# Kernel optimization log

Measured on AMD Instinct MI355X. Metric: run time of the kernel, lower is better.

## Reference

```python
import jax, jax.numpy as jnp
import numpy as np

L = 16          # n_levels
F = 2           # n_features_per_level
LOG2_T = 19
T = 1 << LOG2_T # hashmap size per level
BASE_RES = 16
FINEST_RES = 2048
_b = (FINEST_RES / BASE_RES) ** (1.0 / (L - 1))
RES = [int(np.floor(BASE_RES * _b ** l)) for l in range(L)]
PRIMES = (1, 2654435761, 805459861, 3674653429)
H = 2 * L * F   # 64 = n_neurons (static 32 + dynamic 32)
N_PTS = 2097152


def hash_encode(coords, table):
    """Multi-resolution hash grid encoding. coords [N,D] in [0,1], table [L,T,F] -> [N, L*F]."""
    N, D = coords.shape
    # 2^D corner offsets of the enclosing grid cell
    offsets = np.stack(
        np.meshgrid(*([np.array([0, 1], dtype=np.uint32)] * D), indexing='ij'), -1
    ).reshape(-1, D)
    primes = [jnp.uint32(p) for p in PRIMES[:D]]
    feats = []
    for l in range(L):  # fixed small loop over levels
        pos = coords * RES[l]
        grid = jnp.floor(pos)
        frac = pos - grid                       # [N,D] interpolation weights
        gu = grid.astype(jnp.int32).astype(jnp.uint32)
        acc = jnp.zeros((N, F), coords.dtype)
        for off in offsets:                     # fixed 2^D corners
            idx = gu + off[None, :]
            h = idx[:, 0] * primes[0]
            for d in range(1, D):
                h = h ^ (idx[:, d] * primes[d])
            h = (h & jnp.uint32(T - 1)).astype(jnp.int32)
            w = jnp.prod(jnp.where(off[None, :] != 0, frac, 1.0 - frac), axis=1)
            acc = acc + w[:, None] * table[l, h]
        feats.append(acc)
    return jnp.concatenate(feats, -1)


def setup_inputs() -> dict:
    key = jax.random.key(0)
    ks = jax.random.split(key, 12)
    s = 1.0 / np.sqrt(H)
    return {
        'x': jax.random.uniform(ks[0], (N_PTS, 3), jnp.float32),
        't': jax.random.uniform(ks[1], (), jnp.float32),
        'table_static': jax.random.uniform(ks[2], (L, T, F), jnp.float32, -1e-4, 1e-4),
        'table_dynamic': jax.random.uniform(ks[3], (L, T, F), jnp.float32, -1e-4, 1e-4),
        'w1_0': jax.random.normal(ks[4], (H, H), jnp.float32) * s,
        'w1_1': jax.random.normal(ks[5], (H, H), jnp.float32) * s,
        'w1_2': jax.random.normal(ks[6], (H, H), jnp.float32) * s,
        'w2_0': jax.random.normal(ks[7], (H, H), jnp.float32) * s,
        'w2_1': jax.random.normal(ks[8], (H, H), jnp.float32) * s,
        'w2_2': jax.random.normal(ks[9], (H, 1), jnp.float32) * s,
        'skip_alpha': jnp.float32(0.5),
    }


def reference(x, t, table_static, table_dynamic, w1_0, w1_1, w1_2,
              w2_0, w2_1, w2_2, skip_alpha):
    relu = jax.nn.relu
    # t_input = cat([x, full((N,1), t)])
    t_col = jnp.broadcast_to(t.astype(x.dtype), (x.shape[0], 1))
    t_input = jnp.concatenate([x, t_col], axis=1)
    static_features = hash_encode(x, table_static)          # [N,32]
    dynamic_features = hash_encode(t_input, table_dynamic)  # [N,32]
    feat = jnp.concatenate([static_features, dynamic_features], -1)  # [N,64]
    # net_1: 2 hidden layers, ReLU everywhere incl. output activation
    h = relu(feat @ w1_0)
    h = relu(h @ w1_1)
    out1 = relu(h @ w1_2)
    # adaptive skip blend
    blend = out1 * skip_alpha + (1.0 - skip_alpha) * feat
    # net_2: 2 hidden layers ReLU, linear output -> [N,1]
    h = relu(blend @ w2_0)
    h = relu(h @ w2_1)
    return h @ w2_2
```

## Files before the change

kernel.cpp:

```cpp
#include <hip/hip_runtime.h>
#include <math.h>

#define LVLS 16
#define TMASK ((1u << 19) - 1u)
#define NT 256
#define TSLICE (1u << 20)
#define KPL (1u << 19)

typedef _Float16 h4 __attribute__((ext_vector_type(4)));
typedef short bf8i __attribute__((ext_vector_type(8)));
typedef float f4 __attribute__((ext_vector_type(4)));

#define ESCALE 1024.0f
#define EINV   0.0009765625f

struct ResParams { float rf[LVLS]; };

__device__ __forceinline__ unsigned hash3(unsigned ux, unsigned uy, unsigned uz) {
    return ux ^ (uy * 2654435761u) ^ (uz * 805459861u);
}

__device__ __forceinline__ unsigned short bf16_rne(float f) {
    unsigned u = __builtin_bit_cast(unsigned, f);
    unsigned r = (u + 0x7FFFu + ((u >> 16) & 1u)) >> 16;
    return (unsigned short)r;
}
__device__ __forceinline__ float bf16_to_f(unsigned short h) {
    unsigned u = ((unsigned)h) << 16;
    return __builtin_bit_cast(float, u);
}

__device__ __forceinline__ void split8t(const float* v, bf8i& h, bf8i& l) {
    unsigned H[4], L[4];
    #pragma unroll
    for (int p = 0; p < 4; ++p) {
        const unsigned u0 = __builtin_bit_cast(unsigned, v[2 * p]);
        const unsigned u1 = __builtin_bit_cast(unsigned, v[2 * p + 1]);
        const unsigned h0 = u0 & 0xffff0000u;
        const unsigned h1 = u1 & 0xffff0000u;
        const float l0 = v[2 * p]     - __builtin_bit_cast(float, h0);
        const float l1 = v[2 * p + 1] - __builtin_bit_cast(float, h1);
        H[p] = (u0 >> 16) | h1;
        L[p] = (__builtin_bit_cast(unsigned, l0) >> 16)
             | (__builtin_bit_cast(unsigned, l1) & 0xffff0000u);
    }
    uint4 Hv = make_uint4(H[0], H[1], H[2], H[3]);
    uint4 Lv = make_uint4(L[0], L[1], L[2], L[3]);
    h = __builtin_bit_cast(bf8i, Hv);
    l = __builtin_bit_cast(bf8i, Lv);
}

__global__ __launch_bounds__(NT, 8)
void build_E(const float* __restrict__ tabs, const float* __restrict__ tabd,
             const float* __restrict__ t_ptr, h4* __restrict__ E, ResParams rp)
{
    const unsigned idx = blockIdx.x * NT + threadIdx.x;
    const unsigned l = idx >> 19;
    const unsigned k = idx & TMASK;
    const float r = rp.rf[l];
    const float tt = t_ptr[0];
    const float ft = tt * r;
    const float gt = floorf(ft);
    const float wt = ft - gt;
    const unsigned ut = (unsigned)(int)gt;
    const unsigned c0 = (ut * 3674653429u) & TMASK;
    const unsigned c1 = ((ut + 1u) * 3674653429u) & TMASK;
    const float* ts = tabs + (size_t)l * TSLICE;
    const float* td = tabd + (size_t)l * TSLICE;
    const float2 s  = *(const float2*)(ts + (size_t)k * 2u);
    const float2 d0 = *(const float2*)(td + (size_t)(k ^ c0) * 2u);
    const float2 d1 = *(const float2*)(td + (size_t)(k ^ c1) * 2u);
    const float om = 1.f - wt;
    h4 v;
    v.x = (_Float16)(s.x * ESCALE);
    v.y = (_Float16)(s.y * ESCALE);
    v.z = (_Float16)((om * d0.x + wt * d1.x) * ESCALE);
    v.w = (_Float16)((om * d0.y + wt * d1.y) * ESCALE);
    E[idx] = v;
}

__global__ __launch_bounds__(NT)
void build_W(const float* __restrict__ w10, const float* __restrict__ w11,
             const float* __restrict__ w12, const float* __restrict__ w20,
             const float* __restrict__ w21, const float* __restrict__ w22,
             unsigned short* __restrict__ Wf)
{
    const int tid = blockIdx.x * NT + threadIdx.x;
    if (tid >= 6 * 4 * 2 * 64) return;
    const int lane = tid & 63;
    const int ks = (tid >> 6) & 1;
    const int nt = (tid >> 7) & 3;
    const int L  = tid >> 9;
    const int g = lane >> 4, c = lane & 15;
    unsigned short* dst = Wf + (size_t)tid * 16;
    #pragma unroll
    for (int j = 0; j < 8; ++j) {
        const int k = ks * 32 + g * 8 + j;
        float v;
        if      (L == 0) v = w10[k * 64 + nt * 16 + c];
        else if (L == 1) v = w11[k * 64 + nt * 16 + c];
        else if (L == 2) v = w12[k * 64 + nt * 16 + c];
        else if (L == 3) v = w20[k * 64 + nt * 16 + c];
        else if (L == 4) v = w21[k * 64 + nt * 16 + c];
        else             v = (nt == 0 && c == 0) ? w22[k] : 0.f;
        unsigned short hb = bf16_rne(v);
        unsigned short lb = bf16_rne(v - bf16_to_f(hb));
        dst[j]     = hb;
        dst[8 + j] = lb;
    }
}

__global__ __launch_bounds__(NT, 8)
void enc_all(const float* __restrict__ x, const h4* __restrict__ E,
             h4* __restrict__ fb, long cp, int npts, ResParams rp)
{
    const int b = blockIdx.x;
    const int l = b & 15;
    const int gid = (b >> 4) * NT + threadIdx.x;
    if (gid >= npts) return;
    const float r = rp.rf[l];
    const h4* Es = E + (size_t)l * KPL;

    const float px = x[3 * gid + 0];
    const float py = x[3 * gid + 1];
    const float pz = x[3 * gid + 2];
    const float fx = px * r, fy = py * r, fz = pz * r;
    const float gx = floorf(fx), gy = floorf(fy), gz = floorf(fz);
    const float wx = fx - gx, wy = fy - gy, wz = fz - gz;
    const unsigned ux = (unsigned)(int)gx;
    const unsigned uy = (unsigned)(int)gy;
    const unsigned uz = (unsigned)(int)gz;
    float a0 = 0.f, a1 = 0.f, b0 = 0.f, b1 = 0.f;
    #pragma unroll
    for (int cc = 0; cc < 8; ++cc) {
        const unsigned ox = (cc >> 2) & 1, oy = (cc >> 1) & 1, oz = cc & 1;
        const unsigned kk = hash3(ux + ox, uy + oy, uz + oz) & TMASK;
        const float w = (ox ? wx : 1.f - wx)
                      * (oy ? wy : 1.f - wy)
                      * (oz ? wz : 1.f - wz);
        const h4 e = Es[kk];
        a0 = fmaf(w, (float)e.x, a0);
        a1 = fmaf(w, (float)e.y, a1);
        b0 = fmaf(w, (float)e.z, b0);
        b1 = fmaf(w, (float)e.w, b1);
    }
    h4 v;
    v.x = (_Float16)a0;
    v.y = (_Float16)a1;
    v.z = (_Float16)b0;
    v.w = (_Float16)b1;
    __builtin_nontemporal_store(__builtin_bit_cast(unsigned long long, v),
                                (unsigned long long*)&fb[(size_t)l * cp + gid]);
}

#define MLPT 128
__global__ __launch_bounds__(MLPT)
void mlp_mfma(const h4* __restrict__ fb, long cp, const uint4* __restrict__ Wf,
              const float* __restrict__ alpha_ptr, float* __restrict__ out, int npts)
{
    __shared__ float XBs[2][64 * 68];
    const int lane = threadIdx.x & 63;
    const int wv   = threadIdx.x >> 6;
    const int base = blockIdx.x * MLPT + wv * 64;
    if (base >= npts) return;
    float* xb = XBs[wv];
    const int g = lane >> 4, c = lane & 15;
    const float alpha = alpha_ptr[0];
    const float oma = 1.f - alpha;

    bf8i ah[4][2], al[4][2];

    #pragma unroll
    for (int mt = 0; mt < 4; ++mt) {
        float t0[8], t1[8];
        #pragma unroll
        for (int jj = 0; jj < 4; ++jj) {
            const h4 e = fb[(size_t)(g * 4 + jj) * cp + base + mt * 16 + c];
            t0[2 * jj] = (float)e.x; t0[2 * jj + 1] = (float)e.y;
            t1[2 * jj] = (float)e.z; t1[2 * jj + 1] = (float)e.w;
        }
        split8t(t0, ah[mt][0], al[mt][0]);
        split8t(t1, ah[mt][1], al[mt][1]);
    }

    auto run_layer = [&](int Lidx, bool relu) {
        #pragma unroll
        for (int nt = 0; nt < 4; ++nt) {
            const uint4* wp0 = Wf + ((size_t)(((Lidx * 4 + nt) * 2 + 0) * 64 + lane)) * 2;
            const uint4* wp1 = Wf + ((size_t)(((Lidx * 4 + nt) * 2 + 1) * 64 + lane)) * 2;
            const bf8i wh0 = __builtin_bit_cast(bf8i, wp0[0]);
            const bf8i wl0 = __builtin_bit_cast(bf8i, wp0[1]);
            const bf8i wh1 = __builtin_bit_cast(bf8i, wp1[0]);
            const bf8i wl1 = __builtin_bit_cast(bf8i, wp1[1]);
            f4 acc[4];
            #pragma unroll
            for (int mt = 0; mt < 4; ++mt) acc[mt] = (f4){0.f, 0.f, 0.f, 0.f};
            #pragma unroll
            for (int mt = 0; mt < 4; ++mt)
                acc[mt] = __builtin_amdgcn_mfma_f32_16x16x32_bf16(ah[mt][0], wh0, acc[mt], 0, 0, 0);
            #pragma unroll
            for (int mt = 0; mt < 4; ++mt)
                acc[mt] = __builtin_amdgcn_mfma_f32_16x16x32_bf16(ah[mt][1], wh1, acc[mt], 0, 0, 0);
            #pragma unroll
            for (int mt = 0; mt < 4; ++mt)
                acc[mt] = __builtin_amdgcn_mfma_f32_16x16x32_bf16(ah[mt][0], wl0, acc[mt], 0, 0, 0);
            #pragma unroll
            for (int mt = 0; mt < 4; ++mt)
                acc[mt] = __builtin_amdgcn_mfma_f32_16x16x32_bf16(ah[mt][1], wl1, acc[mt], 0, 0, 0);
            #pragma unroll
            for (int mt = 0; mt < 4; ++mt)
                acc[mt] = __builtin_amdgcn_mfma_f32_16x16x32_bf16(al[mt][0], wh0, acc[mt], 0, 0, 0);
            #pragma unroll
            for (int mt = 0; mt < 4; ++mt)
                acc[mt] = __builtin_amdgcn_mfma_f32_16x16x32_bf16(al[mt][1], wh1, acc[mt], 0, 0, 0);
            #pragma unroll
            for (int mt = 0; mt < 4; ++mt)
              #pragma unroll
              for (int r = 0; r < 4; ++r) {
                float v = acc[mt][r];
                if (relu) v = fmaxf(v, 0.f);
                xb[(mt * 16 + g * 4 + r) * 68 + nt * 16 + c] = v;
              }
        }
    };

    auto load_frags = [&](bool blend) {
        asm volatile("s_waitcnt lgkmcnt(0)" ::: "memory");
        #pragma unroll
        for (int mt = 0; mt < 4; ++mt) {
            float t0[8], t1[8];
            #pragma unroll
            for (int j = 0; j < 8; ++j) t0[j] = xb[(mt * 16 + c) * 68 + g * 8 + j];
            #pragma unroll
            for (int j = 0; j < 8; ++j) t1[j] = xb[(mt * 16 + c) * 68 + 32 + g * 8 + j];
            if (blend) {
                #pragma unroll
                for (int jj = 0; jj < 4; ++jj) {
                    const h4 e = fb[(size_t)(g * 4 + jj) * cp + base + mt * 16 + c];
                    t0[2 * jj]     = fmaf(t0[2 * jj],     alpha, oma * (float)e.x);
                    t0[2 * jj + 1] = fmaf(t0[2 * jj + 1], alpha, oma * (float)e.y);
                    t1[2 * jj]     = fmaf(t1[2 * jj],     alpha, oma * (float)e.z);
                    t1[2 * jj + 1] = fmaf(t1[2 * jj + 1], alpha, oma * (float)e.w);
                }
            }
            split8t(t0, ah[mt][0], al[mt][0]);
            split8t(t1, ah[mt][1], al[mt][1]);
        }
        asm volatile("s_waitcnt lgkmcnt(0)" ::: "memory");
    };

    run_layer(0, true);
    load_frags(false);
    run_layer(1, true);
    load_frags(false);
    run_layer(2, true);
    load_frags(true);
    run_layer(3, true);
    load_frags(false);
    run_layer(4, true);
    load_frags(false);

    {
        const uint4* wp0 = Wf + ((size_t)(((5 * 4 + 0) * 2 + 0) * 64 + lane)) * 2;
        const uint4* wp1 = Wf + ((size_t)(((5 * 4 + 0) * 2 + 1) * 64 + lane)) * 2;
        const bf8i wh0 = __builtin_bit_cast(bf8i, wp0[0]);
        const bf8i wl0 = __builtin_bit_cast(bf8i, wp0[1]);
        const bf8i wh1 = __builtin_bit_cast(bf8i, wp1[0]);
        const bf8i wl1 = __builtin_bit_cast(bf8i, wp1[1]);
        f4 acc[4];
        #pragma unroll
        for (int mt = 0; mt < 4; ++mt) acc[mt] = (f4){0.f, 0.f, 0.f, 0.f};
        #pragma unroll
        for (int mt = 0; mt < 4; ++mt)
            acc[mt] = __builtin_amdgcn_mfma_f32_16x16x32_bf16(ah[mt][0], wh0, acc[mt], 0, 0, 0);
        #pragma unroll
        for (int mt = 0; mt < 4; ++mt)
            acc[mt] = __builtin_amdgcn_mfma_f32_16x16x32_bf16(ah[mt][1], wh1, acc[mt], 0, 0, 0);
        #pragma unroll
        for (int mt = 0; mt < 4; ++mt)
            acc[mt] = __builtin_amdgcn_mfma_f32_16x16x32_bf16(ah[mt][0], wl0, acc[mt], 0, 0, 0);
        #pragma unroll
        for (int mt = 0; mt < 4; ++mt)
            acc[mt] = __builtin_amdgcn_mfma_f32_16x16x32_bf16(ah[mt][1], wl1, acc[mt], 0, 0, 0);
        #pragma unroll
        for (int mt = 0; mt < 4; ++mt)
            acc[mt] = __builtin_amdgcn_mfma_f32_16x16x32_bf16(al[mt][0], wh0, acc[mt], 0, 0, 0);
        #pragma unroll
        for (int mt = 0; mt < 4; ++mt)
            acc[mt] = __builtin_amdgcn_mfma_f32_16x16x32_bf16(al[mt][1], wh1, acc[mt], 0, 0, 0);
        if (c == 0) {
            #pragma unroll
            for (int mt = 0; mt < 4; ++mt) {
                float4 st = make_float4(acc[mt][0] * EINV, acc[mt][1] * EINV,
                                        acc[mt][2] * EINV, acc[mt][3] * EINV);
                *reinterpret_cast<float4*>(&out[base + mt * 16 + g * 4]) = st;
            }
        }
    }
}

__global__ __launch_bounds__(NT, 2)
void hashmlp_fused(const float* __restrict__ x, const float* __restrict__ t_ptr,
                   const float* __restrict__ tab_s, const float* __restrict__ tab_d,
                   const float* __restrict__ w10, const float* __restrict__ w11,
                   const float* __restrict__ w12, const float* __restrict__ w20,
                   const float* __restrict__ w21, const float* __restrict__ w22,
                   const float* __restrict__ alpha_ptr, float* __restrict__ out,
                   int n, ResParams rp)
{
    __shared__ float smem[64 * NT];
    const int tid = threadIdx.x;
    const int gid = blockIdx.x * NT + tid;
    if (gid >= n) return;
    const float px = x[3 * gid], py = x[3 * gid + 1], pz = x[3 * gid + 2];
    const float tt = t_ptr[0];
    const float alpha = alpha_ptr[0];
    float feat[64];
    #pragma unroll
    for (int l = 0; l < LVLS; ++l) {
        const float r = rp.rf[l];
        const float fx = px * r, fy = py * r, fz = pz * r;
        const float gx = floorf(fx), gy = floorf(fy), gz = floorf(fz);
        const float wx = fx - gx, wy = fy - gy, wz = fz - gz;
        const unsigned ux = (unsigned)(int)gx, uy = (unsigned)(int)gy, uz = (unsigned)(int)gz;
        const float* tb = tab_s + ((size_t)l << 20);
        float a0 = 0.f, a1 = 0.f;
        #pragma unroll
        for (int cc = 0; cc < 8; ++cc) {
            const unsigned ox = (cc >> 2) & 1, oy = (cc >> 1) & 1, oz = cc & 1;
            const unsigned idx = hash3(ux + ox, uy + oy, uz + oz) & TMASK;
            const float w = (ox ? wx : 1.f - wx) * (oy ? wy : 1.f - wy) * (oz ? wz : 1.f - wz);
            const float2 f = *reinterpret_cast<const float2*>(tb + ((size_t)idx * 2u));
            a0 = fmaf(w, f.x, a0); a1 = fmaf(w, f.y, a1);
        }
        feat[2 * l] = a0; feat[2 * l + 1] = a1;
    }
    #pragma unroll
    for (int l = 0; l < LVLS; ++l) {
        const float r = rp.rf[l];
        const float fx = px * r, fy = py * r, fz = pz * r;
        const float gx = floorf(fx), gy = floorf(fy), gz = floorf(fz);
        const float wx = fx - gx, wy = fy - gy, wz = fz - gz;
        const unsigned ux = (unsigned)(int)gx, uy = (unsigned)(int)gy, uz = (unsigned)(int)gz;
        const float ftp = tt * r;
        const float gt = floorf(ftp);
        const float wtp = ftp - gt;
        const unsigned ut = (unsigned)(int)gt;
        const unsigned ht0 = ut * 3674653429u;
        const unsigned ht1 = (ut + 1u) * 3674653429u;
        const float* tb = tab_d + ((size_t)l << 20);
        float a0 = 0.f, a1 = 0.f;
        #pragma unroll
        for (int cc = 0; cc < 8; ++cc) {
            const unsigned ox = (cc >> 2) & 1, oy = (cc >> 1) & 1, oz = cc & 1;
            const unsigned hs = hash3(ux + ox, uy + oy, uz + oz);
            const float ws = (ox ? wx : 1.f - wx) * (oy ? wy : 1.f - wy) * (oz ? wz : 1.f - wz);
            {
                const unsigned idx = (hs ^ ht0) & TMASK;
                const float w = ws * (1.f - wtp);
                const float2 f = *reinterpret_cast<const float2*>(tb + ((size_t)idx * 2u));
                a0 = fmaf(w, f.x, a0); a1 = fmaf(w, f.y, a1);
            }
            {
                const unsigned idx = (hs ^ ht1) & TMASK;
                const float w = ws * wtp;
                const float2 f = *reinterpret_cast<const float2*>(tb + ((size_t)idx * 2u));
                a0 = fmaf(w, f.x, a0); a1 = fmaf(w, f.y, a1);
            }
        }
        feat[32 + 2 * l] = a0; feat[33 + 2 * l] = a1;
    }
    #pragma unroll
    for (int i = 0; i < 64; ++i) smem[i * NT + tid] = feat[i];
    float acc[64];
    auto layer = [&](const float* __restrict__ W, bool do_relu) {
        #pragma unroll
        for (int j = 0; j < 64; ++j) acc[j] = 0.f;
        for (int i = 0; i < 64; ++i) {
            const float fi = smem[i * NT + tid];
            const float* wr = W + i * 64;
            #pragma unroll
            for (int j = 0; j < 64; ++j) acc[j] = fmaf(fi, wr[j], acc[j]);
        }
        #pragma unroll
        for (int j = 0; j < 64; ++j) {
            const float v = do_relu ? fmaxf(acc[j], 0.f) : acc[j];
            smem[j * NT + tid] = v;
        }
    };
    layer(w10, true); layer(w11, true); layer(w12, true);
    #pragma unroll
    for (int j = 0; j < 64; ++j) {
        const float o1 = smem[j * NT + tid];
        smem[j * NT + tid] = fmaf(o1, alpha, (1.f - alpha) * feat[j]);
    }
    layer(w20, true); layer(w21, true);
    float o = 0.f;
    for (int i = 0; i < 64; ++i) o = fmaf(smem[i * NT + tid], w22[i], o);
    out[gid] = o;
}

extern "C" void kernel_launch(void* const* d_in, const int* in_sizes, int n_in,
                              void* d_out, int out_size, void* d_ws, size_t ws_size,
                              hipStream_t stream) {
    (void)n_in; (void)out_size;
    const float* x     = (const float*)d_in[0];
    const float* t     = (const float*)d_in[1];
    const float* tabs  = (const float*)d_in[2];
    const float* tabd  = (const float*)d_in[3];
    const float* w10   = (const float*)d_in[4];
    const float* w11   = (const float*)d_in[5];
    const float* w12   = (const float*)d_in[6];
    const float* w20   = (const float*)d_in[7];
    const float* w21   = (const float*)d_in[8];
    const float* w22   = (const float*)d_in[9];
    const float* alpha = (const float*)d_in[10];
    float* out = (float*)d_out;
    const int n = in_sizes[0] / 3;

    ResParams rp;
    const double b = pow(2048.0 / 16.0, 1.0 / 15.0);
    for (int l = 0; l < LVLS; ++l)
        rp.rf[l] = (float)(int)floor(16.0 * pow(b, (double)l));

    const size_t E_BYTES = (size_t)LVLS * KPL * 8u;
    const size_t W_BYTES = 128u * 1024u;
    if (ws_size < E_BYTES + W_BYTES + 256u * 1024u) {
        dim3 grid((n + NT - 1) / NT), block(NT);
        hipLaunchKernelGGL(hashmlp_fused, grid, block, 0, stream,
                           x, t, tabs, tabd, w10, w11, w12, w20, w21, w22,
                           alpha, out, n, rp);
        return;
    }

    h4* E = (h4*)d_ws;
    unsigned short* Wf = (unsigned short*)((char*)d_ws + E_BYTES);
    h4* fb = (h4*)((char*)d_ws + E_BYTES + W_BYTES);
    long cp_cap = (long)((ws_size - E_BYTES - W_BYTES) / 128u) & ~255L;
    long cp = cp_cap < (long)n ? cp_cap : (long)n;

    {
        const unsigned total = LVLS * KPL;
        hipLaunchKernelGGL(build_E, dim3(total / NT), dim3(NT), 0, stream,
                           tabs, tabd, t, E, rp);
        hipLaunchKernelGGL(build_W, dim3(12), dim3(NT), 0, stream,
                           w10, w11, w12, w20, w21, w22, Wf);
    }

    for (long start = 0; start < n; start += cp) {
        const long m = (n - start) < cp ? (n - start) : cp;
        const unsigned ptb = (unsigned)((m + NT - 1) / NT);
        hipLaunchKernelGGL(enc_all, dim3(ptb * 16), dim3(NT), 0, stream,
                           x + 3 * start, E, fb, cp, (int)m, rp);
        dim3 mgrid((unsigned)((m + MLPT - 1) / MLPT));
        hipLaunchKernelGGL(mlp_mfma, mgrid, dim3(MLPT), 0, stream,
                           fb, cp, (const uint4*)Wf, alpha, out + start, (int)m);
    }
}
```

Before: 1.673 ms.

## Process MLP rows in half tiles to shrink LDS; launch encoding level-major

The MLP layer loop now processes the 64-row wave tile in two 32-row halves. After each half it writes activations to a smaller per-wave LDS buffer and reloads fragments, which halves shared memory per block and adds a min-blocks launch bound to raise occupancy. The encode kernel switches from interleaving levels in blockIdx.x to a 2D grid with the level in blockIdx.y. That makes consecutive blocks share a level, which changes hash-table cache locality: better per-level L2 reuse, but possibly worse reuse of x. Splitting into halves adds extra waitcnt syncs and may shorten MFMA dependency chains.

```diff
diff --git a/kernel.cpp b/kernel.cpp
--- a/kernel.cpp
+++ b/kernel.cpp
@@ -114,9 +114,8 @@
 void enc_all(const float* __restrict__ x, const h4* __restrict__ E,
              h4* __restrict__ fb, long cp, int npts, ResParams rp)
 {
-    const int b = blockIdx.x;
-    const int l = b & 15;
-    const int gid = (b >> 4) * NT + threadIdx.x;
+    const int l = blockIdx.y;
+    const int gid = blockIdx.x * NT + threadIdx.x;
     if (gid >= npts) return;
     const float r = rp.rf[l];
     const h4* Es = E + (size_t)l * KPL;
@@ -154,11 +153,11 @@
 }
 
 #define MLPT 128
-__global__ __launch_bounds__(MLPT)
+__global__ __launch_bounds__(MLPT, 4)
 void mlp_mfma(const h4* __restrict__ fb, long cp, const uint4* __restrict__ Wf,
               const float* __restrict__ alpha_ptr, float* __restrict__ out, int npts)
 {
-    __shared__ float XBs[2][64 * 68];
+    __shared__ float XBs[2][32 * 68];
     const int lane = threadIdx.x & 63;
     const int wv   = threadIdx.x >> 6;
     const int base = blockIdx.x * MLPT + wv * 64;
@@ -183,82 +182,69 @@
         split8t(t1, ah[mt][1], al[mt][1]);
     }
 
-    auto run_layer = [&](int Lidx, bool relu) {
-        #pragma unroll
-        for (int nt = 0; nt < 4; ++nt) {
-            const uint4* wp0 = Wf + ((size_t)(((Lidx * 4 + nt) * 2 + 0) * 64 + lane)) * 2;
-            const uint4* wp1 = Wf + ((size_t)(((Lidx * 4 + nt) * 2 + 1) * 64 + lane)) * 2;
-            const bf8i wh0 = __builtin_bit_cast(bf8i, wp0[0]);
-            const bf8i wl0 = __builtin_bit_cast(bf8i, wp0[1]);
-            const bf8i wh1 = __builtin_bit_cast(bf8i, wp1[0]);
-            const bf8i wl1 = __builtin_bit_cast(bf8i, wp1[1]);
-            f4 acc[4];
+    auto layer = [&](int Lidx, bool blend) {
+        #pragma unroll
+        for (int half = 0; half < 2; ++half) {
+            const int m0 = 2 * half, m1 = 2 * half + 1;
             #pragma unroll
-            for (int mt = 0; mt < 4; ++mt) acc[mt] = (f4){0.f, 0.f, 0.f, 0.f};
-            #pragma unroll
-            for (int mt = 0; mt < 4; ++mt)
-                acc[mt] = __builtin_amdgcn_mfma_f32_16x16x32_bf16(ah[mt][0], wh0, acc[mt], 0, 0, 0);
-            #pragma unroll
-            for (int mt = 0; mt < 4; ++mt)
-                acc[mt] = __builtin_amdgcn_mfma_f32_16x16x32_bf16(ah[mt][1], wh1, acc[mt], 0, 0, 0);
-            #pragma unroll
-            for (int mt = 0; mt < 4; ++mt)
-                acc[mt] = __builtin_amdgcn_mfma_f32_16x16x32_bf16(ah[mt][0], wl0, acc[mt], 0, 0, 0);
-            #pragma unroll
-            for (int mt = 0; mt < 4; ++mt)
-                acc[mt] = __builtin_amdgcn_mfma_f32_16x16x32_bf16(ah[mt][1], wl1, acc[mt], 0, 0, 0);
-            #pragma unroll
-            for (int mt = 0; mt < 4; ++mt)
-                acc[mt] = __builtin_amdgcn_mfma_f32_16x16x32_bf16(al[mt][0], wh0, acc[mt], 0, 0, 0);
-            #pragma unroll
-            for (int mt = 0; mt < 4; ++mt)
-                acc[mt] = __builtin_amdgcn_mfma_f32_16x16x32_bf16(al[mt][1], wh1, acc[mt], 0, 0, 0);
-            #pragma unroll
-            for (int mt = 0; mt < 4; ++mt)
-              #pragma unroll
-              for (int r = 0; r < 4; ++r) {
-                float v = acc[mt][r];
-                if (relu) v = fmaxf(v, 0.f);
-                xb[(mt * 16 + g * 4 + r) * 68 + nt * 16 + c] = v;
-              }
-        }
-    };
-
-    auto load_frags = [&](bool blend) {
-        asm volatile("s_waitcnt lgkmcnt(0)" ::: "memory");
-        #pragma unroll
-        for (int mt = 0; mt < 4; ++mt) {
-            float t0[8], t1[8];
-            #pragma unroll
-            for (int j = 0; j < 8; ++j) t0[j] = xb[(mt * 16 + c) * 68 + g * 8 + j];
-            #pragma unroll
-            for (int j = 0; j < 8; ++j) t1[j] = xb[(mt * 16 + c) * 68 + 32 + g * 8 + j];
-            if (blend) {
+            for (int nt = 0; nt < 4; ++nt) {
+                const uint4* wp0 = Wf + ((size_t)(((Lidx * 4 + nt) * 2 + 0) * 64 + lane)) * 2;
+                const uint4* wp1 = Wf + ((size_t)(((Lidx * 4 + nt) * 2 + 1) * 64 + lane)) * 2;
+                const bf8i wh0 = __builtin_bit_cast(bf8i, wp0[0]);
+                const bf8i wl0 = __builtin_bit_cast(bf8i, wp0[1]);
+                const bf8i wh1 = __builtin_bit_cast(bf8i, wp1[0]);
+                const bf8i wl1 = __builtin_bit_cast(bf8i, wp1[1]);
+                f4 acc0 = (f4){0.f, 0.f, 0.f, 0.f};
+                f4 acc1 = (f4){0.f, 0.f, 0.f, 0.f};
+                acc0 = __builtin_amdgcn_mfma_f32_16x16x32_bf16(ah[m0][0], wh0, acc0, 0, 0, 0);
+                acc1 = __builtin_amdgcn_mfma_f32_16x16x32_bf16(ah[m1][0], wh0, acc1, 0, 0, 0);
+                acc0 = __builtin_amdgcn_mfma_f32_16x16x32_bf16(ah[m0][1], wh1, acc0, 0, 0, 0);
+                acc1 = __builtin_amdgcn_mfma_f32_16x16x32_bf16(ah[m1][1], wh1, acc1, 0, 0, 0);
+                acc0 = __builtin_amdgcn_mfma_f32_16x16x32_bf16(ah[m0][0], wl0, acc0, 0, 0, 0);
+                acc1 = __builtin_amdgcn_mfma_f32_16x16x32_bf16(ah[m1][0], wl0, acc1, 0, 0, 0);
+                acc0 = __builtin_amdgcn_mfma_f32_16x16x32_bf16(ah[m0][1], wl1, acc0, 0, 0, 0);
+                acc1 = __builtin_amdgcn_mfma_f32_16x16x32_bf16(ah[m1][1], wl1, acc1, 0, 0, 0);
+                acc0 = __builtin_amdgcn_mfma_f32_16x16x32_bf16(al[m0][0], wh0, acc0, 0, 0, 0);
+                acc1 = __builtin_amdgcn_mfma_f32_16x16x32_bf16(al[m1][0], wh0, acc1, 0, 0, 0);
+                acc0 = __builtin_amdgcn_mfma_f32_16x16x32_bf16(al[m0][1], wh1, acc0, 0, 0, 0);
+                acc1 = __builtin_amdgcn_mfma_f32_16x16x32_bf16(al[m1][1], wh1, acc1, 0, 0, 0);
                 #pragma unroll
-                for (int jj = 0; jj < 4; ++jj) {
-                    const h4 e = fb[(size_t)(g * 4 + jj) * cp + base + mt * 16 + c];
-                    t0[2 * jj]     = fmaf(t0[2 * jj],     alpha, oma * (float)e.x);
-                    t0[2 * jj + 1] = fmaf(t0[2 * jj + 1], alpha, oma * (float)e.y);
-                    t1[2 * jj]     = fmaf(t1[2 * jj],     alpha, oma * (float)e.z);
-                    t1[2 * jj + 1] = fmaf(t1[2 * jj + 1], alpha, oma * (float)e.w);
+                for (int r = 0; r < 4; ++r) {
+                    xb[(0 * 16 + g * 4 + r) * 68 + nt * 16 + c] = fmaxf(acc0[r], 0.f);
+                    xb[(1 * 16 + g * 4 + r) * 68 + nt * 16 + c] = fmaxf(acc1[r], 0.f);
                 }
             }
-            split8t(t0, ah[mt][0], al[mt][0]);
-            split8t(t1, ah[mt][1], al[mt][1]);
-        }
-        asm volatile("s_waitcnt lgkmcnt(0)" ::: "memory");
+            asm volatile("s_waitcnt lgkmcnt(0)" ::: "memory");
+            #pragma unroll
+            for (int q = 0; q < 2; ++q) {
+                const int mt = 2 * half + q;
+                float t0[8], t1[8];
+                #pragma unroll
+                for (int j = 0; j < 8; ++j) t0[j] = xb[(q * 16 + c) * 68 + g * 8 + j];
+                #pragma unroll
+                for (int j = 0; j < 8; ++j) t1[j] = xb[(q * 16 + c) * 68 + 32 + g * 8 + j];
+                if (blend) {
+                    #pragma unroll
+                    for (int jj = 0; jj < 4; ++jj) {
+                        const h4 e = fb[(size_t)(g * 4 + jj) * cp + base + mt * 16 + c];
+                        t0[2 * jj]     = fmaf(t0[2 * jj],     alpha, oma * (float)e.x);
+                        t0[2 * jj + 1] = fmaf(t0[2 * jj + 1], alpha, oma * (float)e.y);
+                        t1[2 * jj]     = fmaf(t1[2 * jj],     alpha, oma * (float)e.z);
+                        t1[2 * jj + 1] = fmaf(t1[2 * jj + 1], alpha, oma * (float)e.w);
+                    }
+                }
+                split8t(t0, ah[mt][0], al[mt][0]);
+                split8t(t1, ah[mt][1], al[mt][1]);
+            }
+            asm volatile("s_waitcnt lgkmcnt(0)" ::: "memory");
+        }
     };
 
-    run_layer(0, true);
-    load_frags(false);
-    run_layer(1, true);
-    load_frags(false);
-    run_layer(2, true);
-    load_frags(true);
-    run_layer(3, true);
-    load_frags(false);
-    run_layer(4, true);
-    load_frags(false);
+    layer(0, false);
+    layer(1, false);
+    layer(2, true);
+    layer(3, false);
+    layer(4, false);
 
     {
         const uint4* wp0 = Wf + ((size_t)(((5 * 4 + 0) * 2 + 0) * 64 + lane)) * 2;
@@ -449,8 +435,8 @@
 
     for (long start = 0; start < n; start += cp) {
         const long m = (n - start) < cp ? (n - start) : cp;
-        const unsigned ptb = (unsigned)((m + NT - 1) / NT);
-        hipLaunchKernelGGL(enc_all, dim3(ptb * 16), dim3(NT), 0, stream,
+        dim3 egrid((unsigned)((m + NT - 1) / NT), LVLS);
+        hipLaunchKernelGGL(enc_all, egrid, dim3(NT), 0, stream,
                            x + 3 * start, E, fb, cp, (int)m, rp);
         dim3 mgrid((unsigned)((m + MLPT - 1) / MLPT));
         hipLaunchKernelGGL(mlp_mfma, mgrid, dim3(MLPT), 0, stream,
```

Result: faster. 1.381 ms, median of 2 (-17.4%).
